# Optimization experiments

Hardware: AMD Instinct MI355X
Metric: run time of the kernel (lower is better)

## Reference

```python
import jax, jax.numpy as jnp
import numpy as np

N_NODES = 100000
N_EDGES = 1600000
D = 64
NUM_GROUPS = 2


def setup_inputs() -> dict:
    key = jax.random.key(0)
    k_h, k_ws, k_wg, k_src, k_dst, k_grp = jax.random.split(key, 6)
    h = jax.random.normal(k_h, (N_NODES, D), dtype=jnp.float32)
    # nn.Linear(in, out, bias=False) weights have shape [out, in]
    W_self = jax.random.normal(k_ws, (D, D), dtype=jnp.float32) * (1.0 / np.sqrt(D))
    W_groups = jax.random.normal(k_wg, (NUM_GROUPS, D, D), dtype=jnp.float32) * (1.0 / np.sqrt(D))
    src = jax.random.randint(k_src, (N_EDGES,), 0, N_NODES, dtype=jnp.int32)
    dst = jax.random.randint(k_dst, (N_EDGES,), 0, N_NODES, dtype=jnp.int32)
    group_labels = jax.random.randint(k_grp, (N_NODES,), 0, NUM_GROUPS, dtype=jnp.int32)
    return {"h": h, "W_self": W_self, "W_groups": W_groups,
            "src": src, "dst": dst, "group_labels": group_labels}


def reference(h, W_self, W_groups, src, dst, group_labels):
    # h: [N, d_in]; W_self: [d_out, d_in]; W_groups: [G, d_out, d_in]
    # Edge list (src, dst) replaces the DGL graph; message m_e = h[src_e],
    # transformed by W_groups[group[src_e]], scatter-added into dst_e.
    n_nodes = h.shape[0]
    num_groups = W_groups.shape[0]

    h_self = h @ W_self.T                       # [N, d_out]

    h_src = jnp.take(h, src, axis=0)            # [E, d_in] edge gather
    g_src = jnp.take(group_labels, src, axis=0)  # [E]

    h_agg = jnp.zeros((n_nodes, W_groups.shape[1]), dtype=h.dtype)
    for i in range(num_groups):  # small fixed loop over groups
        masked = jnp.where((g_src == i)[:, None], h_src, 0.0)  # [E, d_in]
        # Linearity lets us aggregate first, then transform (same math as
        # transforming each message then scatter_add, but far less compute).
        seg = jax.ops.segment_sum(masked, dst, num_segments=n_nodes)  # [N, d_in]
        h_agg = h_agg + seg @ W_groups[i].T      # [N, d_out]

    return h_self + h_agg
```

## Files before the change

kernel.cpp:

```cpp
#include <hip/hip_runtime.h>

#define N_NODES 100000
#define N_EDGES 1600000
#define D 64
#define NB 196
#define NR 8
#define CAPB_R 1280
#define LCAP 64
#define SRC_MASK 0x1FFFF

typedef unsigned int u32;
typedef short bfrag8 __attribute__((ext_vector_type(8)));
typedef float f32x4 __attribute__((ext_vector_type(4)));


__device__ inline u32 pk_bf16(float lo, float hi) {
    u32 a = __float_as_uint(lo);
    a = (a + 0x7fffu + ((a >> 16) & 1u)) >> 16;
    u32 b = __float_as_uint(hi);
    b = (b + 0x7fffu + ((b >> 16) & 1u)) & 0xffff0000u;
    return a | b;
}

__global__ __launch_bounds__(256) void transcode(const float* __restrict__ h,
                                                 const float* __restrict__ W_self,
                                                 const float* __restrict__ W_groups,
                                                 u32* __restrict__ X,
                                                 u32* __restrict__ Wc) {
    if (blockIdx.x < 12500) {
        int i = blockIdx.x * 256 + threadIdx.x;
        int n = i >> 5, c = i & 31;
        float2 v = reinterpret_cast<const float2*>(h)[i];
        X[(size_t)n * 96 + c] = pk_bf16(v.x, v.y);
    } else {
        for (int idx = threadIdx.x; idx < 6144; idx += 256) {
            int j = idx / 96, kk = idx - j * 96;
            int k = kk * 2;
            float lo, hi;
            if (k < 64)       { lo = W_self[j * 64 + k];          hi = W_self[j * 64 + k + 1]; }
            else if (k < 128) { lo = W_groups[j * 64 + k - 64];   hi = W_groups[j * 64 + k - 63]; }
            else              { lo = W_groups[4096 + j * 64 + k - 128];
                                hi = W_groups[4096 + j * 64 + k - 127]; }
            Wc[j * 96 + kk] = pk_bf16(lo, hi);
        }
    }
}

__global__ __launch_bounds__(256) void bucket_edges(const int* __restrict__ src,
                                                    const int* __restrict__ dst,
                                                    const int* __restrict__ grp,
                                                    int* __restrict__ bcnt,
                                                    int* __restrict__ buckets) {
    __shared__ int hist[NB];
    __shared__ int gbase[NB];
    const int tid = threadIdx.x;
    const int r = blockIdx.x & (NR - 1);
    for (int b = tid; b < NB; b += 256) hist[b] = 0;
    __syncthreads();

    int ent[8], bkt[8], rnk[8];
    const int e0 = blockIdx.x * 2048;
#pragma unroll
    for (int i = 0; i < 8; ++i) {
        int e = e0 + tid + i * 256;
        if (e < N_EDGES) {
            int s = src[e], d = dst[e];
            int g = grp[s];
            bkt[i] = d >> 9;
            ent[i] = s | (g << 17) | ((d & 511) << 18);
            rnk[i] = atomicAdd(&hist[bkt[i]], 1);
        } else {
            bkt[i] = -1;
        }
    }
    __syncthreads();
    for (int b = tid; b < NB; b += 256) {
        int hc = hist[b];
        gbase[b] = hc ? atomicAdd(&bcnt[b * NR + r], hc) : 0;
    }
    __syncthreads();
#pragma unroll
    for (int i = 0; i < 8; ++i) {
        if (bkt[i] >= 0) {
            int pos = gbase[bkt[i]] + rnk[i];
            if (pos < CAPB_R)
                buckets[(bkt[i] * NR + r) * CAPB_R + pos] = ent[i];
        }
    }
}

__global__ __launch_bounds__(256) void gather(u32* X,
                                              const int* __restrict__ bcnt,
                                              const int* __restrict__ buckets) {
    __shared__ int lcsr[64 * LCAP];
    __shared__ int cnt0[64];
    __shared__ int cnt1[64];

    const int tid = threadIdx.x;
    const int cb = blockIdx.x >> 3;
    const int sub = blockIdx.x & 7;
    const int nbase = cb * 512 + sub * 64;
    if (nbase >= N_NODES) return;

    if (tid < 64) { cnt0[tid] = 0; cnt1[tid] = 0; }
    __syncthreads();

    for (int r = 0; r < NR; ++r) {
        const int cnt = min(bcnt[cb * NR + r], CAPB_R);
        const int* bp = buckets + (cb * NR + r) * CAPB_R;
        for (int i = tid; i < cnt; i += 256) {
            int e = bp[i];
            int doff = (e >> 18) & 511;
            if ((doff >> 6) == sub) {
                int nl = doff & 63;
                if ((e >> 17) & 1) {
                    int s1 = atomicAdd(&cnt1[nl], 1);
                    if (s1 < LCAP) lcsr[nl * LCAP + (LCAP - 1 - s1)] = e;
                } else {
                    int s0 = atomicAdd(&cnt0[nl], 1);
                    if (s0 < LCAP) lcsr[nl * LCAP + s0] = e;
                }
            }
        }
    }
    __syncthreads();

    const int wave = tid >> 6;
    const int lane = tid & 63;
    const int half = lane >> 5;
    const int c = lane & 31;

    for (int q = 0; q < 16; ++q) {
        const int nl = wave * 16 + q;
        const int n = nbase + nl;
        if (n >= N_NODES) continue;

        const int c0 = min(cnt0[nl], LCAP);
        const int c1 = min(cnt1[nl], LCAP);
        float a0l = 0.f, a0h = 0.f, a1l = 0.f, a1h = 0.f;

        for (int i = 0; i < c0; i += 8) {
#pragma unroll
            for (int k = 0; k < 4; ++k) {
                int t = i + 2 * k + half;
                bool ok = t < c0;
                int e = lcsr[nl * LCAP + min(t, LCAP - 1)];
                u32 v = X[(size_t)(e & SRC_MASK) * 96 + c];
                a0l += ok ? __uint_as_float(v << 16) : 0.f;
                a0h += ok ? __uint_as_float(v & 0xffff0000u) : 0.f;
            }
        }
        for (int i = 0; i < c1; i += 8) {
#pragma unroll
            for (int k = 0; k < 4; ++k) {
                int t = i + 2 * k + half;
                bool ok = t < c1;
                int e = lcsr[nl * LCAP + (LCAP - 1 - min(t, LCAP - 1))];
                u32 v = X[(size_t)(e & SRC_MASK) * 96 + c];
                a1l += ok ? __uint_as_float(v << 16) : 0.f;
                a1h += ok ? __uint_as_float(v & 0xffff0000u) : 0.f;
            }
        }

        a0l += __shfl_xor(a0l, 32, 64);
        a0h += __shfl_xor(a0h, 32, 64);
        a1l += __shfl_xor(a1l, 32, 64);
        a1h += __shfl_xor(a1h, 32, 64);

        if (half == 0) {
            X[(size_t)n * 96 + 32 + c] = pk_bf16(a0l, a0h);
            X[(size_t)n * 96 + 64 + c] = pk_bf16(a1l, a1h);
        }
    }
}

__global__ __launch_bounds__(256) void gemm_mfma(const u32* __restrict__ X,
                                                 const u32* __restrict__ Wc,
                                                 float* __restrict__ out) {
    const int tid = threadIdx.x;
    const int wave = tid >> 6;
    const int lane = tid & 63;
    const int m = lane & 15;
    const int quad = lane >> 4;
    const int n0 = blockIdx.x * 64 + wave * 16;

    int arow = n0 + m;
    if (arow > N_NODES - 1) arow = N_NODES - 1;

    union Cvt { uint4 u; bfrag8 s; };

    bfrag8 a[6];
    const u32* ap = X + (size_t)arow * 96 + quad * 4;
#pragma unroll
    for (int ks = 0; ks < 6; ++ks) {
        Cvt cv;
        cv.u = *reinterpret_cast<const uint4*>(ap + ks * 16);
        a[ks] = cv.s;
    }

    f32x4 acc[4];
#pragma unroll
    for (int jt = 0; jt < 4; ++jt) acc[jt] = (f32x4){0.f, 0.f, 0.f, 0.f};

    const u32* wp = Wc + (size_t)m * 96 + quad * 4;
#pragma unroll
    for (int ks = 0; ks < 6; ++ks) {
#pragma unroll
        for (int jt = 0; jt < 4; ++jt) {
            Cvt cw;
            cw.u = *reinterpret_cast<const uint4*>(wp + jt * 1536 + ks * 16);
            acc[jt] = __builtin_amdgcn_mfma_f32_16x16x32_bf16(a[ks], cw.s, acc[jt], 0, 0, 0);
        }
    }

    const int rbase = n0 + quad * 4;
#pragma unroll
    for (int jt = 0; jt < 4; ++jt) {
#pragma unroll
        for (int r = 0; r < 4; ++r) {
            int n = rbase + r;
            if (n < N_NODES)
                out[(size_t)n * 64 + jt * 16 + m] = acc[jt][r];
        }
    }
}

extern "C" void kernel_launch(void* const* d_in, const int* in_sizes, int n_in,
                              void* d_out, int out_size, void* d_ws, size_t ws_size,
                              hipStream_t stream) {
    const float* h        = (const float*)d_in[0];
    const float* W_self   = (const float*)d_in[1];
    const float* W_groups = (const float*)d_in[2];
    const int*   src      = (const int*)d_in[3];
    const int*   dst      = (const int*)d_in[4];
    const int*   grp      = (const int*)d_in[5];
    float*       out      = (float*)d_out;

    int* bcnt    = (int*)d_ws;
    int* buckets = bcnt + 2048;
    u32* X       = (u32*)(buckets + NB * NR * CAPB_R);
    u32* Wc      = X + (size_t)N_NODES * 96;

    hipMemsetAsync(bcnt, 0, NB * NR * sizeof(int), stream);

    transcode<<<12501, 256, 0, stream>>>(h, W_self, W_groups, X, Wc);
    bucket_edges<<<(N_EDGES + 2047) / 2048, 256, 0, stream>>>(src, dst, grp, bcnt, buckets);
    gather<<<NB * NR, 256, 0, stream>>>(X, bcnt, buckets);
    gemm_mfma<<<(N_NODES + 63) / 64, 256, 0, stream>>>(X, Wc, out);
}
```

Before: 207.6 us.

## Fuse transcode and edge bucketing into one prep kernel; halve gather block size

Merges the transcode and bucket_edges kernels into a single prep launch, with bucketing blocks placed first so they overlap with the transcode work and one kernel launch is saved. The gather kernel now handles 32 nodes per block instead of 64 and launches twice as many blocks. It stores precomputed row offsets in shared memory and splits each gather loop into unmasked full iterations plus a masked tail. This aims to cut launch overhead, raise occupancy, and trim per-edge index arithmetic. In exchange, each bucket is rescanned by 16 blocks rather than 8, which adds bucket-read traffic.

New measurement: 214.3 us. 3.2% more time.

```diff
diff --git a/kernel.cpp b/kernel.cpp
--- a/kernel.cpp
+++ b/kernel.cpp
@@ -8,6 +8,7 @@
 #define CAPB_R 1280
 #define LCAP 64
 #define SRC_MASK 0x1FFFF
+#define NBB 782
 
 typedef unsigned int u32;
 typedef short bfrag8 __attribute__((ext_vector_type(8)));
@@ -22,18 +23,62 @@
     return a | b;
 }
 
-__global__ __launch_bounds__(256) void transcode(const float* __restrict__ h,
-                                                 const float* __restrict__ W_self,
-                                                 const float* __restrict__ W_groups,
-                                                 u32* __restrict__ X,
-                                                 u32* __restrict__ Wc) {
-    if (blockIdx.x < 12500) {
-        int i = blockIdx.x * 256 + threadIdx.x;
+__global__ __launch_bounds__(256) void prep(const float* __restrict__ h,
+                                            const float* __restrict__ W_self,
+                                            const float* __restrict__ W_groups,
+                                            const int* __restrict__ src,
+                                            const int* __restrict__ dst,
+                                            const int* __restrict__ grp,
+                                            int* __restrict__ bcnt,
+                                            int* __restrict__ buckets,
+                                            u32* __restrict__ X,
+                                            u32* __restrict__ Wc) {
+    __shared__ int hist[NB];
+    __shared__ int gbase[NB];
+    const int tid = threadIdx.x;
+    const int bx = blockIdx.x;
+
+    if (bx < NBB) {
+        const int r = bx & (NR - 1);
+        for (int b = tid; b < NB; b += 256) hist[b] = 0;
+        __syncthreads();
+
+        int ent[8], bkt[8], rnk[8];
+        const int e0 = bx * 2048;
+#pragma unroll
+        for (int i = 0; i < 8; ++i) {
+            int e = e0 + tid + i * 256;
+            if (e < N_EDGES) {
+                int s = src[e], d = dst[e];
+                int g = grp[s];
+                bkt[i] = d >> 9;
+                ent[i] = s | (g << 17) | ((d & 511) << 18);
+                rnk[i] = atomicAdd(&hist[bkt[i]], 1);
+            } else {
+                bkt[i] = -1;
+            }
+        }
+        __syncthreads();
+        for (int b = tid; b < NB; b += 256) {
+            int hc = hist[b];
+            gbase[b] = hc ? atomicAdd(&bcnt[b * NR + r], hc) : 0;
+        }
+        __syncthreads();
+#pragma unroll
+        for (int i = 0; i < 8; ++i) {
+            if (bkt[i] >= 0) {
+                int pos = gbase[bkt[i]] + rnk[i];
+                if (pos < CAPB_R)
+                    buckets[(bkt[i] * NR + r) * CAPB_R + pos] = ent[i];
+            }
+        }
+    } else if (bx < NBB + 12500) {
+        int i = (bx - NBB) * 256 + tid;
         int n = i >> 5, c = i & 31;
         float2 v = reinterpret_cast<const float2*>(h)[i];
         X[(size_t)n * 96 + c] = pk_bf16(v.x, v.y);
     } else {
-        for (int idx = threadIdx.x; idx < 6144; idx += 256) {
+        for (int idx = tid; idx < 6144; idx += 256) {
             int j = idx / 96, kk = idx - j * 96;
             int k = kk * 2;
             float lo, hi;
@@ -46,63 +91,20 @@
     }
 }
 
-__global__ __launch_bounds__(256) void bucket_edges(const int* __restrict__ src,
-                                                    const int* __restrict__ dst,
-                                                    const int* __restrict__ grp,
-                                                    int* __restrict__ bcnt,
-                                                    int* __restrict__ buckets) {
-    __shared__ int hist[NB];
-    __shared__ int gbase[NB];
-    const int tid = threadIdx.x;
-    const int r = blockIdx.x & (NR - 1);
-    for (int b = tid; b < NB; b += 256) hist[b] = 0;
-    __syncthreads();
-
-    int ent[8], bkt[8], rnk[8];
-    const int e0 = blockIdx.x * 2048;
-#pragma unroll
-    for (int i = 0; i < 8; ++i) {
-        int e = e0 + tid + i * 256;
-        if (e < N_EDGES) {
-            int s = src[e], d = dst[e];
-            int g = grp[s];
-            bkt[i] = d >> 9;
-            ent[i] = s | (g << 17) | ((d & 511) << 18);
-            rnk[i] = atomicAdd(&hist[bkt[i]], 1);
-        } else {
-            bkt[i] = -1;
-        }
-    }
-    __syncthreads();
-    for (int b = tid; b < NB; b += 256) {
-        int hc = hist[b];
-        gbase[b] = hc ? atomicAdd(&bcnt[b * NR + r], hc) : 0;
-    }
-    __syncthreads();
-#pragma unroll
-    for (int i = 0; i < 8; ++i) {
-        if (bkt[i] >= 0) {
-            int pos = gbase[bkt[i]] + rnk[i];
-            if (pos < CAPB_R)
-                buckets[(bkt[i] * NR + r) * CAPB_R + pos] = ent[i];
-        }
-    }
-}
-
 __global__ __launch_bounds__(256) void gather(u32* X,
                                               const int* __restrict__ bcnt,
                                               const int* __restrict__ buckets) {
-    __shared__ int lcsr[64 * LCAP];
-    __shared__ int cnt0[64];
-    __shared__ int cnt1[64];
+    __shared__ int lcsr[32 * LCAP];
+    __shared__ int cnt0[32];
+    __shared__ int cnt1[32];
 
     const int tid = threadIdx.x;
-    const int cb = blockIdx.x >> 3;
-    const int sub = blockIdx.x & 7;
-    const int nbase = cb * 512 + sub * 64;
+    const int cb = blockIdx.x >> 4;
+    const int sub = blockIdx.x & 15;
+    const int nbase = cb * 512 + sub * 32;
     if (nbase >= N_NODES) return;
 
-    if (tid < 64) { cnt0[tid] = 0; cnt1[tid] = 0; }
+    if (tid < 32) { cnt0[tid] = 0; cnt1[tid] = 0; }
     __syncthreads();
 
     for (int r = 0; r < NR; ++r) {
@@ -110,15 +112,15 @@
         const int* bp = buckets + (cb * NR + r) * CAPB_R;
         for (int i = tid; i < cnt; i += 256) {
             int e = bp[i];
-            int doff = (e >> 18) & 511;
-            if ((doff >> 6) == sub) {
-                int nl = doff & 63;
+            if (((e >> 23) & 15) == sub) {
+                int nl = (e >> 18) & 31;
+                int off = (e & SRC_MASK) * 96;
                 if ((e >> 17) & 1) {
                     int s1 = atomicAdd(&cnt1[nl], 1);
-                    if (s1 < LCAP) lcsr[nl * LCAP + (LCAP - 1 - s1)] = e;
+                    if (s1 < LCAP) lcsr[nl * LCAP + (LCAP - 1 - s1)] = off;
                 } else {
                     int s0 = atomicAdd(&cnt0[nl], 1);
-                    if (s0 < LCAP) lcsr[nl * LCAP + s0] = e;
+                    if (s0 < LCAP) lcsr[nl * LCAP + s0] = off;
                 }
             }
         }
@@ -130,33 +132,53 @@
     const int half = lane >> 5;
     const int c = lane & 31;
 
-    for (int q = 0; q < 16; ++q) {
-        const int nl = wave * 16 + q;
+    for (int q = 0; q < 8; ++q) {
+        const int nl = wave * 8 + q;
         const int n = nbase + nl;
         if (n >= N_NODES) continue;
 
         const int c0 = min(cnt0[nl], LCAP);
         const int c1 = min(cnt1[nl], LCAP);
+        const int full0 = c0 & ~7;
+        const int full1 = c1 & ~7;
         float a0l = 0.f, a0h = 0.f, a1l = 0.f, a1h = 0.f;
 
-        for (int i = 0; i < c0; i += 8) {
-#pragma unroll
-            for (int k = 0; k < 4; ++k) {
-                int t = i + 2 * k + half;
+        for (int i = 0; i < full0; i += 8) {
+#pragma unroll
+            for (int k = 0; k < 4; ++k) {
+                int off = lcsr[nl * LCAP + i + 2 * k + half];
+                u32 v = X[(size_t)off + c];
+                a0l += __uint_as_float(v << 16);
+                a0h += __uint_as_float(v & 0xffff0000u);
+            }
+        }
+        if (full0 < c0) {
+#pragma unroll
+            for (int k = 0; k < 4; ++k) {
+                int t = full0 + 2 * k + half;
                 bool ok = t < c0;
-                int e = lcsr[nl * LCAP + min(t, LCAP - 1)];
-                u32 v = X[(size_t)(e & SRC_MASK) * 96 + c];
+                int off = ok ? lcsr[nl * LCAP + t] : 0;
+                u32 v = X[(size_t)off + c];
                 a0l += ok ? __uint_as_float(v << 16) : 0.f;
                 a0h += ok ? __uint_as_float(v & 0xffff0000u) : 0.f;
             }
         }
-        for (int i = 0; i < c1; i += 8) {
-#pragma unroll
-            for (int k = 0; k < 4; ++k) {
-                int t = i + 2 * k + half;
+        for (int i = 0; i < full1; i += 8) {
+#pragma unroll
+            for (int k = 0; k < 4; ++k) {
+                int off = lcsr[nl * LCAP + (LCAP - 1 - (i + 2 * k + half))];
+                u32 v = X[(size_t)off + c];
+                a1l += __uint_as_float(v << 16);
+                a1h += __uint_as_float(v & 0xffff0000u);
+            }
+        }
+        if (full1 < c1) {
+#pragma unroll
+            for (int k = 0; k < 4; ++k) {
+                int t = full1 + 2 * k + half;
                 bool ok = t < c1;
-                int e = lcsr[nl * LCAP + (LCAP - 1 - min(t, LCAP - 1))];
-                u32 v = X[(size_t)(e & SRC_MASK) * 96 + c];
+                int off = ok ? lcsr[nl * LCAP + (LCAP - 1 - t)] : 0;
+                u32 v = X[(size_t)off + c];
                 a1l += ok ? __uint_as_float(v << 16) : 0.f;
                 a1h += ok ? __uint_as_float(v & 0xffff0000u) : 0.f;
             }
@@ -243,8 +265,8 @@
 
     hipMemsetAsync(bcnt, 0, NB * NR * sizeof(int), stream);
 
-    transcode<<<12501, 256, 0, stream>>>(h, W_self, W_groups, X, Wc);
-    bucket_edges<<<(N_EDGES + 2047) / 2048, 256, 0, stream>>>(src, dst, grp, bcnt, buckets);
-    gather<<<NB * NR, 256, 0, stream>>>(X, bcnt, buckets);
+    prep<<<NBB + 12500 + 1, 256, 0, stream>>>(h, W_self, W_groups, src, dst, grp,
+                                              bcnt, buckets, X, Wc);
+    gather<<<NB * 16, 256, 0, stream>>>(X, bcnt, buckets);
     gemm_mfma<<<(N_NODES + 63) / 64, 256, 0, stream>>>(X, Wc, out);
 }
```
